# Performance work log

Hardware: AMD Instinct MI355X
Metric: run time of the kernel (lower is better)

The kernel has to match this reference:

```python
import jax, jax.numpy as jnp
import numpy as np

EMBED_DIM = 768
NUM_HEADS = 12
HEAD_DIM = EMBED_DIM // NUM_HEADS
SCALE = HEAD_DIM ** -0.5


def setup_inputs() -> dict:
    key = jax.random.key(0)
    k1, k2, k3, k4, k5 = jax.random.split(key, 5)
    B, T = 8, 1024
    hidden_states = jax.random.normal(k1, (B, T, EMBED_DIM), dtype=jnp.float32)
    init = 0.02
    qkv_w = jax.random.normal(k2, (EMBED_DIM, 3 * EMBED_DIM), dtype=jnp.float32) * init
    qkv_b = jnp.zeros((3 * EMBED_DIM,), dtype=jnp.float32)
    proj_w = jax.random.normal(k3, (EMBED_DIM, EMBED_DIM), dtype=jnp.float32) * init
    proj_b = jnp.zeros((EMBED_DIM,), dtype=jnp.float32)
    return {
        "hidden_states": hidden_states,
        "qkv_w": qkv_w,
        "qkv_b": qkv_b,
        "proj_w": proj_w,
        "proj_b": proj_b,
    }


def reference(hidden_states, qkv_w, qkv_b, proj_w, proj_b):
    B, T, C = hidden_states.shape
    # fused QKV projection
    mixed = hidden_states @ qkv_w + qkv_b            # [B, T, 3C]
    mixed = mixed.reshape(B, T, 3, NUM_HEADS, HEAD_DIM)
    mixed = jnp.transpose(mixed, (2, 0, 3, 1, 4))    # [3, B, H, T, D]
    q, k, v = mixed[0], mixed[1], mixed[2]
    # scaled dot-product attention (dropout is identity in eval)
    scores = jnp.einsum("bhqd,bhkd->bhqk", q, k) * SCALE
    probs = jax.nn.softmax(scores, axis=-1)
    ctx = jnp.einsum("bhqk,bhkd->bhqd", probs, v)    # [B, H, T, D]
    ctx = jnp.transpose(ctx, (0, 2, 1, 3)).reshape(B, T, C)
    out = ctx @ proj_w + proj_b
    return out
```

## Files before the change

kernel.cpp:

```cpp
#include <hip/hip_runtime.h>

#define EMBED 768
#define NHEAD 12
#define HDIM 64
#define BATCH 8
#define SEQ 1024
#define ROWS (BATCH*SEQ)
#define QKVN (3*EMBED)
#define ATTN_SCALE 0.125f

typedef short s16x8 __attribute__((ext_vector_type(8)));
typedef short s16x4 __attribute__((ext_vector_type(4)));
typedef float f32x4 __attribute__((ext_vector_type(4)));

__device__ __forceinline__ float bf2f(unsigned short u) {
    union { unsigned int i; float f; } v; v.i = ((unsigned int)u) << 16; return v.f;
}
__device__ __forceinline__ unsigned short f2bf(float f) {
    unsigned int i = __builtin_bit_cast(unsigned int, f);
    i += 0x7FFFu + ((i >> 16) & 1u);
    return (unsigned short)(i >> 16);
}

__device__ __forceinline__ void async16(short* lds, const unsigned short* g) {
    __builtin_amdgcn_global_load_lds(
        (const __attribute__((address_space(1))) unsigned int*)g,
        (__attribute__((address_space(3))) unsigned int*)lds,
        16, 0, 0);
}

__device__ __forceinline__ f32x4 mfma16(s16x4 a, s16x4 b, f32x4 c) {
#if __has_builtin(__builtin_amdgcn_mfma_f32_16x16x16bf16_1k)
    return __builtin_amdgcn_mfma_f32_16x16x16bf16_1k(a, b, c, 0, 0, 0);
#else
    asm volatile("v_mfma_f32_16x16x16_bf16 %0, %1, %2, %0" : "+v"(c) : "v"(a), "v"(b));
    return c;
#endif
}

__global__ __launch_bounds__(256) void prep_k(
    const float* __restrict__ qkv_w, unsigned short* __restrict__ WqkvT,
    const float* __restrict__ proj_w, unsigned short* __restrict__ WprojT,
    const float* __restrict__ hidden, unsigned short* __restrict__ hiddenBf)
{
    __shared__ float tile[64][65];
    int blk = blockIdx.x;
    int t = threadIdx.x;
    if (blk < 576) {
        const float* in; unsigned short* outp; int K, N, tx, ty;
        if (blk < 432) { in = qkv_w; outp = WqkvT; K = EMBED; N = QKVN; tx = blk % 36; ty = blk / 36; }
        else { int b2 = blk - 432; in = proj_w; outp = WprojT; K = EMBED; N = EMBED; tx = b2 % 12; ty = b2 / 12; }
        int n0 = tx * 64, k0 = ty * 64;
        int c = t & 63, r0 = t >> 6;
        #pragma unroll
        for (int i = 0; i < 16; i++) {
            int r = r0 * 16 + i;
            tile[r][c] = in[(long long)(k0 + r) * N + n0 + c];
        }
        __syncthreads();
        #pragma unroll
        for (int i = 0; i < 16; i++) {
            int nr = r0 * 16 + i;
            outp[(long long)(n0 + nr) * K + k0 + c] = f2bf(tile[c][nr]);
        }
    } else {
        int tid = (blk - 576) * 256 + t;
        int base = tid * 8;
        float4 f0 = *(const float4*)&hidden[base];
        float4 f1 = *(const float4*)&hidden[base + 4];
        s16x8 a;
        a[0] = (short)f2bf(f0.x); a[1] = (short)f2bf(f0.y);
        a[2] = (short)f2bf(f0.z); a[3] = (short)f2bf(f0.w);
        a[4] = (short)f2bf(f1.x); a[5] = (short)f2bf(f1.y);
        a[6] = (short)f2bf(f1.z); a[7] = (short)f2bf(f1.w);
        *(s16x8*)&hiddenBf[base] = a;
    }
}

template <int OUT_F32>
__global__ __launch_bounds__(256) void gemm128(
    const unsigned short* __restrict__ A,
    const unsigned short* __restrict__ Bt,
    const float* __restrict__ bias,
    void* __restrict__ Cv,
    int M, int N, int K)
{
    __shared__ short As[2][128 * 32];
    __shared__ short Bs[2][128 * 32];
    int t = threadIdx.x, lane = t & 63, w = t >> 6;
    int quad = lane >> 4, low = lane & 15;
    int orig = blockIdx.y * gridDim.x + blockIdx.x;
    int xcd = orig & 7;
    int local = orig >> 3;
    int bx = xcd * 8 + (local & 7);
    int by = local >> 3;
    int m0 = bx * 128, n0 = by * 128;
    int wm = (w & 1) * 64, wn = (w >> 1) * 64;

    int ci0 = w * 128 + lane;
    int r0 = ci0 >> 2, c0 = (ci0 & 3) ^ ((r0 >> 1) & 3);
    int ci1 = ci0 + 64;
    int r1 = ci1 >> 2, c1 = (ci1 & 3) ^ ((r1 >> 1) & 3);
    const unsigned short* pa0 = A + (long long)(m0 + r0) * K + c0 * 8;
    const unsigned short* pa1 = A + (long long)(m0 + r1) * K + c1 * 8;
    const unsigned short* pb0 = Bt + (long long)(n0 + r0) * K + c0 * 8;
    const unsigned short* pb1 = Bt + (long long)(n0 + r1) * K + c1 * 8;
    int lo0 = (w * 128) * 8;
    int lo1 = (w * 128 + 64) * 8;

    async16(&As[0][lo0], pa0);
    async16(&As[0][lo1], pa1);
    async16(&Bs[0][lo0], pb0);
    async16(&Bs[0][lo1], pb1);
    __syncthreads();

    f32x4 acc[4][4] = {};
    int cur = 0;
    for (int k0 = 0; k0 < K; k0 += 32) {
        int nxt = cur ^ 1;
        if (k0 + 32 < K) {
            async16(&As[nxt][lo0], pa0 + k0 + 32);
            async16(&As[nxt][lo1], pa1 + k0 + 32);
            async16(&Bs[nxt][lo0], pb0 + k0 + 32);
            async16(&Bs[nxt][lo1], pb1 + k0 + 32);
        }
        const short* as = As[cur];
        const short* bs = Bs[cur];
        s16x8 af[4], bfr[4];
        #pragma unroll
        for (int i = 0; i < 4; i++) {
            int ra = wm + i * 16 + low;
            af[i] = *(const s16x8*)&as[ra * 32 + ((quad ^ ((ra >> 1) & 3)) * 8)];
            int rb = wn + i * 16 + low;
            bfr[i] = *(const s16x8*)&bs[rb * 32 + ((quad ^ ((rb >> 1) & 3)) * 8)];
        }
        #pragma unroll
        for (int i = 0; i < 4; i++)
            #pragma unroll
            for (int j = 0; j < 4; j++)
                acc[i][j] = __builtin_amdgcn_mfma_f32_16x16x32_bf16(af[i], bfr[j], acc[i][j], 0, 0, 0);
        __syncthreads();
        cur = nxt;
    }
    #pragma unroll
    for (int i = 0; i < 4; i++)
        #pragma unroll
        for (int j = 0; j < 4; j++)
            #pragma unroll
            for (int r = 0; r < 4; r++) {
                int m = m0 + wm + i * 16 + quad * 4 + r;
                int n = n0 + wn + j * 16 + low;
                float v = acc[i][j][r] + bias[n];
                if (OUT_F32) ((float*)Cv)[(long long)m * N + n] = v;
                else ((unsigned short*)Cv)[(long long)m * N + n] = f2bf(v);
            }
}

__global__ __launch_bounds__(256) void attn_k(
    const unsigned short* __restrict__ mixed,
    unsigned short* __restrict__ ctx)
{
    __shared__ short Ks[64 * 64];
    __shared__ short Vt[64 * 68];
    int blk = blockIdx.x;
    int bh = blk % 96;
    int qc = blk / 96;
    int b = bh / NHEAD, h = bh - b * NHEAD;
    int t = threadIdx.x;
    int lane = t & 63, w = t >> 6;
    int quad = lane >> 4, low = lane & 15;
    long long rowbase = (long long)b * SEQ;
    int q0 = qc * 128 + w * 32;
    int hoff = h * HDIM;

    s16x8 qf[2][2];
    #pragma unroll
    for (int qh = 0; qh < 2; qh++) {
        long long r = (rowbase + q0 + qh * 16 + low) * QKVN + hoff;
        qf[qh][0] = *(const s16x8*)&mixed[r + quad * 8];
        qf[qh][1] = *(const s16x8*)&mixed[r + 32 + quad * 8];
    }

    int s0 = w * 128 + lane;
    int kr0 = s0 >> 3, kc0 = s0 & 7;
    int kg = kc0 ^ (kr0 & 7);
    const unsigned short* pk0 = mixed + (rowbase + kr0) * QKVN + EMBED + hoff + kg * 8;
    const unsigned short* pk1 = mixed + (rowbase + kr0 + 8) * QKVN + EMBED + hoff + kg * 8;
    short* lk0 = Ks + (w * 128) * 8;
    short* lk1 = Ks + (w * 128 + 64) * 8;

    int dblk = t & 15, rq = t >> 4;
    const unsigned short* pv = mixed + (rowbase + rq * 4) * QKVN + 2 * EMBED + hoff + dblk * 4;

    f32x4 o[2][4] = {};
    float lsum[2] = {0.f, 0.f};

    for (int kv0 = 0; kv0 < SEQ; kv0 += 64) {
        long long koff = (long long)kv0 * QKVN;
        __syncthreads();
        async16(lk0, pk0 + koff);
        async16(lk1, pk1 + koff);
        s16x4 v0 = *(const s16x4*)&pv[koff];
        s16x4 v1 = *(const s16x4*)&pv[koff + QKVN];
        s16x4 v2 = *(const s16x4*)&pv[koff + 2 * QKVN];
        s16x4 v3 = *(const s16x4*)&pv[koff + 3 * QKVN];
        #pragma unroll
        for (int k = 0; k < 4; k++) {
            s16x4 wv;
            wv[0] = v0[k]; wv[1] = v1[k]; wv[2] = v2[k]; wv[3] = v3[k];
            *(s16x4*)&Vt[(dblk * 4 + k) * 68 + rq * 4] = wv;
        }
        __syncthreads();

        f32x4 sT[2][4] = {};
        __builtin_amdgcn_s_setprio(1);
        #pragma unroll
        for (int n = 0; n < 4; n++) {
            int rr = n * 16 + low;
            int key = low & 7;
            s16x8 kf0 = *(const s16x8*)&Ks[rr * 64 + ((quad ^ key) * 8)];
            s16x8 kf1 = *(const s16x8*)&Ks[rr * 64 + (((quad + 4) ^ key) * 8)];
            sT[0][n] = __builtin_amdgcn_mfma_f32_16x16x32_bf16(kf0, qf[0][0], sT[0][n], 0, 0, 0);
            sT[0][n] = __builtin_amdgcn_mfma_f32_16x16x32_bf16(kf1, qf[0][1], sT[0][n], 0, 0, 0);
            sT[1][n] = __builtin_amdgcn_mfma_f32_16x16x32_bf16(kf0, qf[1][0], sT[1][n], 0, 0, 0);
            sT[1][n] = __builtin_amdgcn_mfma_f32_16x16x32_bf16(kf1, qf[1][1], sT[1][n], 0, 0, 0);
        }
        __builtin_amdgcn_s_setprio(0);

        s16x4 pf[2][4];
        #pragma unroll
        for (int qh = 0; qh < 2; qh++)
            #pragma unroll
            for (int n = 0; n < 4; n++) {
                float e0 = __expf(sT[qh][n][0] * ATTN_SCALE);
                float e1 = __expf(sT[qh][n][1] * ATTN_SCALE);
                float e2 = __expf(sT[qh][n][2] * ATTN_SCALE);
                float e3 = __expf(sT[qh][n][3] * ATTN_SCALE);
                lsum[qh] += (e0 + e1) + (e2 + e3);
                unsigned int w0, w1;
                asm("v_cvt_pk_bf16_f32 %0, %1, %2" : "=v"(w0) : "v"(e0), "v"(e1));
                asm("v_cvt_pk_bf16_f32 %0, %1, %2" : "=v"(w1) : "v"(e2), "v"(e3));
                union { unsigned int u[2]; s16x4 v; } pu;
                pu.u[0] = w0; pu.u[1] = w1;
                pf[qh][n] = pu.v;
            }

        __builtin_amdgcn_s_setprio(1);
        #pragma unroll
        for (int nt = 0; nt < 4; nt++) {
            int drow = nt * 16 + low;
            #pragma unroll
            for (int n = 0; n < 4; n++) {
                s16x4 vf = *(const s16x4*)&Vt[drow * 68 + n * 16 + quad * 4];
                o[0][nt] = mfma16(pf[0][n], vf, o[0][nt]);
                o[1][nt] = mfma16(pf[1][n], vf, o[1][nt]);
            }
        }
        __builtin_amdgcn_s_setprio(0);
    }

    #pragma unroll
    for (int qh = 0; qh < 2; qh++) {
        lsum[qh] += __shfl_xor(lsum[qh], 16, 64);
        lsum[qh] += __shfl_xor(lsum[qh], 32, 64);
    }
    #pragma unroll
    for (int qh = 0; qh < 2; qh++)
        #pragma unroll
        for (int r = 0; r < 4; r++) {
            float inv = 1.0f / __shfl(lsum[qh], quad * 4 + r, 64);
            int q = q0 + qh * 16 + quad * 4 + r;
            #pragma unroll
            for (int nt = 0; nt < 4; nt++)
                ctx[(rowbase + q) * EMBED + hoff + nt * 16 + low] =
                    f2bf(o[qh][nt][r] * inv);
        }
}

extern "C" void kernel_launch(void* const* d_in, const int* in_sizes, int n_in,
                              void* d_out, int out_size, void* d_ws, size_t ws_size,
                              hipStream_t stream) {
    const float* hidden = (const float*)d_in[0];
    const float* qkv_w  = (const float*)d_in[1];
    const float* qkv_b  = (const float*)d_in[2];
    const float* proj_w = (const float*)d_in[3];
    const float* proj_b = (const float*)d_in[4];
    float* out = (float*)d_out;

    char* ws = (char*)d_ws;
    unsigned short* hiddenBf = (unsigned short*)ws;
    unsigned short* ctx      = (unsigned short*)ws;
    unsigned short* WqkvT    = (unsigned short*)(ws + 12582912);
    unsigned short* WprojT   = (unsigned short*)(ws + 16121856);
    unsigned short* mixed    = (unsigned short*)(ws + 17301504);

    prep_k<<<dim3(3648), 256, 0, stream>>>(qkv_w, WqkvT, proj_w, WprojT, hidden, hiddenBf);
    gemm128<0><<<dim3(ROWS / 128, QKVN / 128), 256, 0, stream>>>(
        hiddenBf, WqkvT, qkv_b, mixed, ROWS, QKVN, EMBED);
    attn_k<<<dim3(96 * 8), 256, 0, stream>>>(mixed, ctx);
    gemm128<1><<<dim3(ROWS / 128, EMBED / 128), 256, 0, stream>>>(
        ctx, WprojT, proj_b, out, ROWS, EMBED, EMBED);
}
```

Measured before the change: 192.2 us.

## Split attention KV range across two wave gangs and merge partials in LDS

Each attention block now has 512 threads split into two gangs of four waves. Each gang covers the same 128 queries but only half of the 1024 keys, using its own K/V LDS buffers. The gangs then combine their partial outputs and row sums through shared memory before normalising and writing. The goal is more waves in flight and a shorter serial KV loop per wave, at the cost of more LDS per block, an extra reduction step, and a tighter per-thread register budget from the 512-thread launch bound.

```diff
diff --git a/kernel.cpp b/kernel.cpp
--- a/kernel.cpp
+++ b/kernel.cpp
@@ -156,22 +156,26 @@
             }
 }
 
-__global__ __launch_bounds__(256) void attn_k(
+__global__ __launch_bounds__(512) void attn_k(
     const unsigned short* __restrict__ mixed,
     unsigned short* __restrict__ ctx)
 {
-    __shared__ short Ks[64 * 64];
-    __shared__ short Vt[64 * 68];
+    __shared__ __align__(16) char smem[34816];
     int blk = blockIdx.x;
     int bh = blk % 96;
     int qc = blk / 96;
     int b = bh / NHEAD, h = bh - b * NHEAD;
     int t = threadIdx.x;
+    int tl = t & 255;
     int lane = t & 63, w = t >> 6;
+    int wq = w & 3, gang = w >> 2;
     int quad = lane >> 4, low = lane & 15;
     long long rowbase = (long long)b * SEQ;
-    int q0 = qc * 128 + w * 32;
+    int q0 = qc * 128 + wq * 32;
     int hoff = h * HDIM;
+
+    short* Ks = (short*)(smem + gang * 16896);
+    short* Vt = (short*)(smem + gang * 16896 + 8192);
 
     s16x8 qf[2][2];
     #pragma unroll
@@ -181,22 +185,23 @@
         qf[qh][1] = *(const s16x8*)&mixed[r + 32 + quad * 8];
     }
 
-    int s0 = w * 128 + lane;
+    int s0 = wq * 128 + lane;
     int kr0 = s0 >> 3, kc0 = s0 & 7;
     int kg = kc0 ^ (kr0 & 7);
     const unsigned short* pk0 = mixed + (rowbase + kr0) * QKVN + EMBED + hoff + kg * 8;
     const unsigned short* pk1 = mixed + (rowbase + kr0 + 8) * QKVN + EMBED + hoff + kg * 8;
-    short* lk0 = Ks + (w * 128) * 8;
-    short* lk1 = Ks + (w * 128 + 64) * 8;
-
-    int dblk = t & 15, rq = t >> 4;
+    short* lk0 = Ks + (wq * 128) * 8;
+    short* lk1 = Ks + (wq * 128 + 64) * 8;
+
+    int dblk = tl & 15, rq = tl >> 4;
     const unsigned short* pv = mixed + (rowbase + rq * 4) * QKVN + 2 * EMBED + hoff + dblk * 4;
 
     f32x4 o[2][4] = {};
     float lsum[2] = {0.f, 0.f};
 
-    for (int kv0 = 0; kv0 < SEQ; kv0 += 64) {
-        long long koff = (long long)kv0 * QKVN;
+    int kvbase = gang * 512;
+    for (int it = 0; it < 8; it++) {
+        long long koff = (long long)(kvbase + it * 64) * QKVN;
         __syncthreads();
         async16(lk0, pk0 + koff);
         async16(lk1, pk1 + koff);
@@ -264,17 +269,40 @@
         lsum[qh] += __shfl_xor(lsum[qh], 16, 64);
         lsum[qh] += __shfl_xor(lsum[qh], 32, 64);
     }
-    #pragma unroll
-    for (int qh = 0; qh < 2; qh++)
-        #pragma unroll
-        for (int r = 0; r < 4; r++) {
-            float inv = 1.0f / __shfl(lsum[qh], quad * 4 + r, 64);
-            int q = q0 + qh * 16 + quad * 4 + r;
+
+    f32x4* xo = (f32x4*)smem;
+    float*  xl = (float*)(smem + 32768);
+    __syncthreads();
+    if (gang == 1) {
+        #pragma unroll
+        for (int qh = 0; qh < 2; qh++) {
             #pragma unroll
             for (int nt = 0; nt < 4; nt++)
-                ctx[(rowbase + q) * EMBED + hoff + nt * 16 + low] =
-                    f2bf(o[qh][nt][r] * inv);
-        }
+                xo[((wq * 2 + qh) * 4 + nt) * 64 + lane] = o[qh][nt];
+            xl[(wq * 2 + qh) * 64 + lane] = lsum[qh];
+        }
+    }
+    __syncthreads();
+    if (gang == 0) {
+        #pragma unroll
+        for (int qh = 0; qh < 2; qh++) {
+            #pragma unroll
+            for (int nt = 0; nt < 4; nt++)
+                o[qh][nt] += xo[((wq * 2 + qh) * 4 + nt) * 64 + lane];
+            lsum[qh] += xl[(wq * 2 + qh) * 64 + lane];
+        }
+        #pragma unroll
+        for (int qh = 0; qh < 2; qh++)
+            #pragma unroll
+            for (int r = 0; r < 4; r++) {
+                float inv = 1.0f / __shfl(lsum[qh], quad * 4 + r, 64);
+                int q = q0 + qh * 16 + quad * 4 + r;
+                #pragma unroll
+                for (int nt = 0; nt < 4; nt++)
+                    ctx[(rowbase + q) * EMBED + hoff + nt * 16 + low] =
+                        f2bf(o[qh][nt][r] * inv);
+            }
+    }
 }
 
 extern "C" void kernel_launch(void* const* d_in, const int* in_sizes, int n_in,
@@ -297,7 +325,7 @@
     prep_k<<<dim3(3648), 256, 0, stream>>>(qkv_w, WqkvT, proj_w, WprojT, hidden, hiddenBf);
     gemm128<0><<<dim3(ROWS / 128, QKVN / 128), 256, 0, stream>>>(
         hiddenBf, WqkvT, qkv_b, mixed, ROWS, QKVN, EMBED);
-    attn_k<<<dim3(96 * 8), 256, 0, stream>>>(mixed, ctx);
+    attn_k<<<dim3(96 * 8), 512, 0, stream>>>(mixed, ctx);
     gemm128<1><<<dim3(ROWS / 128, EMBED / 128), 256, 0, stream>>>(
         ctx, WprojT, proj_b, out, ROWS, EMBED, EMBED);
 }
```

Result: no change. 190.4 us (-1.0%).
